# Optimization experiments

Measured on AMD Instinct MI355X. Metric: run time of the kernel, lower is better.

## Reference

```python
import jax, jax.numpy as jnp
import numpy as np

B, N, D, L = 16, 100, 1024, 2000


def setup_inputs() -> dict:
    key = jax.random.key(0)
    ks = jax.random.split(key, 9)
    s = 1.0 / np.sqrt(D)
    return {
        "feature": jax.random.normal(ks[0], (B, N, D), dtype=jnp.float32),
        "graph": jax.random.randint(ks[1], (B, N, N), 0, L),
        "W0": jax.random.normal(ks[2], (D, D), dtype=jnp.float32) * s,
        "W1": jax.random.normal(ks[3], (D, D), dtype=jnp.float32) * s,
        "bias": jax.random.uniform(ks[4], (L, D), dtype=jnp.float32, minval=-s, maxval=s),
        "dp_Wa": jax.random.normal(ks[5], (D, D), dtype=jnp.float32) * s,
        "dp_ba": jax.random.normal(ks[6], (D,), dtype=jnp.float32) * s,
        "dp_Wb": jax.random.normal(ks[7], (D, D), dtype=jnp.float32) * s,
        "dp_bb": jax.random.normal(ks[8], (D,), dtype=jnp.float32) * s,
        "get_alpha": 0,
    }


def reference(feature, graph, W0, W1, bias, dp_Wa, dp_ba, dp_Wb, dp_bb, get_alpha):
    # ---- DirectedGraphConv.conv ----
    adj = (graph != 0).astype(feature.dtype)                     # [B,N,N]
    out = feature + feature @ W0.T + feature @ W1.T              # [B,N,D]
    out = out + jnp.take(bias, graph, axis=0).sum(axis=2)        # label-embedding gather+sum over neighbors
    # ---- relation_alpha: DotProduct(feature, feature) ----
    a = feature @ dp_Wa.T + dp_ba                                # [B,N,D]
    b = feature @ dp_Wb.T + dp_bb                                # [B,N,D]
    alpha = jnp.einsum('bik,bjk->bij', a, b)                     # [B,N,N]
    alpha = jnp.maximum(alpha, 0.0)                              # alpha[alpha<0]=0
    alpha = jnp.einsum('bij,bjk->bik', adj, alpha)               # bmm(adj, alpha)
    alpha = jax.nn.softmax(alpha, axis=1)                        # Softmax(dim=1)
    out = jnp.einsum('bij,bjk->bik', alpha, out)                 # bmm(alpha, output)
    if get_alpha:
        return (out, alpha)
    return out
```

## Files before the change

kernel.cpp:

```cpp
#include <hip/hip_runtime.h>
#include <stdint.h>

#define B_   16
#define N_   100
#define D_   1024
#define L_   2000
#define M_   1600
#define KP   2048
#define AK   3072

#define RCAP 24
#define DCAP 32
#define ZMAX 2400
#define TC   6

typedef __bf16 bf16x8 __attribute__((ext_vector_type(8)));
typedef float  f32x4  __attribute__((ext_vector_type(4)));

__device__ __forceinline__ void gl_lds16(const __bf16* g, __bf16* l) {
    __builtin_amdgcn_global_load_lds(
        (const __attribute__((address_space(1))) void*)g,
        (__attribute__((address_space(3))) void*)l, 16, 0, 0);
}


__global__ void __launch_bounds__(256)
k_prep(const float* __restrict__ f,
       const float* __restrict__ W0, const float* __restrict__ W1,
       const float* __restrict__ Wa, const float* __restrict__ Wb,
       const float* __restrict__ bias, const int* __restrict__ graph,
       __bf16* __restrict__ Acat, __bf16* __restrict__ B0cat,
       __bf16* __restrict__ wcat12, int* __restrict__ colZ) {
    int bid = blockIdx.x, t = threadIdx.x;
    __shared__ float lds[32][33];
    __shared__ unsigned int hist[KP];

    if (bid < 2336) {
        int i = bid * 256 + t;
        union { __bf16 h[8]; uint4 u; } pk;
        if (i < 204800) {
            long base = (long)i * 8;
            const float4* p = (const float4*)(f + base);
            float4 x = p[0], y = p[1];
            pk.h[0]=(__bf16)x.x; pk.h[1]=(__bf16)x.y; pk.h[2]=(__bf16)x.z; pk.h[3]=(__bf16)x.w;
            pk.h[4]=(__bf16)y.x; pk.h[5]=(__bf16)y.y; pk.h[6]=(__bf16)y.z; pk.h[7]=(__bf16)y.w;
            int m = i >> 7, c = i & 127;
            ((uint4*)Acat)[(long)m * 384 + c] = pk.u;
        } else {
            int j = i - 204800;
            long base = (long)j * 8;
            long seg = base >> 20;
            int  js  = j & 131071;
            if (seg == 0) {
                long off = (long)js * 8;
                const float4* p0 = (const float4*)(W0 + off);
                const float4* p1 = (const float4*)(W1 + off);
                float4 a0 = p0[0], a1 = p0[1], b0 = p1[0], b1 = p1[1];
                pk.h[0]=(__bf16)(a0.x+b0.x); pk.h[1]=(__bf16)(a0.y+b0.y);
                pk.h[2]=(__bf16)(a0.z+b0.z); pk.h[3]=(__bf16)(a0.w+b0.w);
                pk.h[4]=(__bf16)(a1.x+b1.x); pk.h[5]=(__bf16)(a1.y+b1.y);
                pk.h[6]=(__bf16)(a1.z+b1.z); pk.h[7]=(__bf16)(a1.w+b1.w);
                int row = js >> 7, c = js & 127;
                ((uint4*)B0cat)[(long)row * 384 + c] = pk.u;
            } else {
                const float* src = (seg == 1) ? Wa : Wb;
                long off = (long)js * 8;
                const float4* p = (const float4*)(src + off);
                float4 x = p[0], y = p[1];
                pk.h[0]=(__bf16)x.x; pk.h[1]=(__bf16)x.y; pk.h[2]=(__bf16)x.z; pk.h[3]=(__bf16)x.w;
                pk.h[4]=(__bf16)y.x; pk.h[5]=(__bf16)y.y; pk.h[6]=(__bf16)y.z; pk.h[7]=(__bf16)y.w;
                ((uint4*)wcat12)[(long)(seg - 1) * 131072 + js] = pk.u;
            }
        }
    } else if (bid < 4384) {
        int tb = bid - 2336;
        int lt = tb >> 5, dt = tb & 31;
        int l0 = lt * 32, d0 = dt * 32;
        int r = t >> 3, cq = (t & 7) * 4;
        float4 v = make_float4(0.f, 0.f, 0.f, 0.f);
        if (l0 + r < L_) v = *(const float4*)(bias + (long)(l0 + r) * D_ + d0 + cq);
        lds[r][cq]=v.x; lds[r][cq+1]=v.y; lds[r][cq+2]=v.z; lds[r][cq+3]=v.w;
        __syncthreads();
        union { __bf16 h[4]; uint2 u; } pk;
        #pragma unroll
        for (int q = 0; q < 4; ++q) pk.h[q] = (__bf16)lds[cq + q][r];
        *(uint2*)(B0cat + (long)(d0 + r) * AK + 1024 + l0 + cq) = pk.u;
    } else if (bid < 5984) {
        int m = bid - 4384;
        for (int k = t; k < KP; k += 256) hist[k] = 0u;
        __syncthreads();
        if (t < N_) atomicAdd(&hist[graph[(long)m * N_ + t]], 1u);
        __syncthreads();
        union { __bf16 h[8]; uint4 u; } pk;
        #pragma unroll
        for (int q = 0; q < 8; ++q) pk.h[q] = (__bf16)(float)hist[t * 8 + q];
        ((uint4*)(Acat + (long)m * AK + 1024))[t] = pk.u;
    } else {
        int b = bid - 5984;
        if (t < N_) {
            const int* g = graph + (long)b * N_ * N_;
            int c = 0;
            for (int i = 0; i < N_; ++i) c += (g[i * N_ + t] == 0);
            colZ[b * N_ + t] = c;
        }
    }
}


#define BM 64
#define BN 128
#define BK 64

__global__ void __launch_bounds__(256)
k_gemmAll(const __bf16* __restrict__ Acat, const __bf16* __restrict__ B0cat,
          const __bf16* __restrict__ wcat12, const int* __restrict__ colZ,
          const float* __restrict__ feat, const float* __restrict__ ba,
          const float* __restrict__ bbias,
          float* __restrict__ out0, float* __restrict__ out0b, float* __restrict__ out0c,
          float* __restrict__ bB, float* __restrict__ aD) {
    __shared__ __align__(16) __bf16 As[BM * BK];
    __shared__ __align__(16) __bf16 Bs[BN * BK];
    __shared__ int czL[2 * N_];
    __shared__ int dcolL[2][DCAP];
    int t = threadIdx.x;
    int pid = blockIdx.x;
    int lane = t & 63, wave = t >> 6;
    int wr = wave & 1, wc = wave >> 1;
    int lrow = lane & 15, quad = lane >> 4;

    int kind, chunk = 0, bm, bn;
    long ldb, koff = 0;
    const __bf16 *Bg;
    if (pid < 600) {
        kind = 0; chunk = pid / 200;
        int p = pid - chunk * 200;
        int v = (p & 7) * 25 + (p >> 3);
        bm = v >> 3; bn = v & 7;
        koff = (long)chunk * 1024;
        Bg = B0cat + (long)(bn * BN) * AK + koff;
        ldb = AK;
    } else if (pid < 800) {
        kind = 1;
        int p = pid - 600;
        int v = (p & 7) * 25 + (p >> 3);
        bm = v >> 3; bn = v & 7;
        Bg = wcat12 + (long)(1024 + bn * BN) * 1024;
        ldb = 1024;
    } else {
        kind = 2;
        int p = pid - 800;
        bn = p & 7; bm = p >> 3;
        Bg = wcat12 + (long)(bn * BN) * 1024;
        ldb = 1024;
        if (t < 2 * N_) czL[t] = colZ[bm * 2 * N_ + t];
        __syncthreads();
        if (t < 2) {
            int rank = 0;
            for (int j = 0; j < N_; ++j)
                if (czL[t * N_ + j] > 0 && rank < DCAP) dcolL[t][rank++] = j;
            for (; rank < DCAP; ++rank) dcolL[t][rank] = 0;
        }
        __syncthreads();
    }

    int r0 = t >> 3, r1 = 32 + (t >> 3);
    int c0 = (t & 7) ^ (r0 & 7), c1 = (t & 7) ^ (r1 & 7);
    const __bf16 *aS0, *aS1;
    if (kind == 2) {
        int b0g = bm * 2 + (r0 >> 5), s0 = r0 & 31;
        int b1g = bm * 2 + (r1 >> 5), s1 = r1 & 31;
        aS0 = Acat + (long)(b0g * N_ + dcolL[r0 >> 5][s0]) * AK + c0 * 8;
        aS1 = Acat + (long)(b1g * N_ + dcolL[r1 >> 5][s1]) * AK + c1 * 8;
    } else {
        aS0 = Acat + (long)(bm * BM + r0) * AK + koff + c0 * 8;
        aS1 = Acat + (long)(bm * BM + r1) * AK + koff + c1 * 8;
    }
    const __bf16 *bS[4];
    #pragma unroll
    for (int pi = 0; pi < 4; ++pi) {
        int rb = pi * 32 + (t >> 3), cb = (t & 7) ^ (rb & 7);
        bS[pi] = Bg + (long)rb * ldb + cb * 8;
    }

    f32x4 acc[2][4] = {};
    for (int k0 = 0; k0 < 1024; k0 += BK) {
        gl_lds16(aS0 + k0, As + t * 8);
        gl_lds16(aS1 + k0, As + (256 + t) * 8);
        #pragma unroll
        for (int pi = 0; pi < 4; ++pi)
            gl_lds16(bS[pi] + k0, Bs + (pi * 256 + t) * 8);
        __syncthreads();
        #pragma unroll
        for (int ks = 0; ks < 2; ++ks) {
            bf16x8 af[2], bf[4];
            #pragma unroll
            for (int i = 0; i < 2; ++i) {
                int r = wr * 32 + i * 16 + lrow;
                int slot = r * 8 + (((ks << 2) | quad) ^ (r & 7));
                af[i] = *(const bf16x8*)(As + slot * 8);
            }
            #pragma unroll
            for (int j = 0; j < 4; ++j) {
                int r = wc * 64 + j * 16 + lrow;
                int slot = r * 8 + (((ks << 2) | quad) ^ (r & 7));
                bf[j] = *(const bf16x8*)(Bs + slot * 8);
            }
            #pragma unroll
            for (int i = 0; i < 2; ++i)
                #pragma unroll
                for (int j = 0; j < 4; ++j)
                    acc[i][j] = __builtin_amdgcn_mfma_f32_16x16x32_bf16(af[i], bf[j], acc[i][j], 0, 0, 0);
        }
        __syncthreads();
    }

    #pragma unroll
    for (int i = 0; i < 2; ++i) {
        int gm0 = bm * BM + wr * 32 + i * 16 + quad * 4;
        #pragma unroll
        for (int j = 0; j < 4; ++j) {
            int col = bn * BN + wc * 64 + j * 16 + lrow;
            #pragma unroll
            for (int r = 0; r < 4; ++r) {
                long m = gm0 + r;
                float v = acc[i][j][r];
                if (kind == 0) {
                    if (chunk == 0)      out0[m * D_ + col]  = v + feat[m * D_ + col];
                    else if (chunk == 1) out0b[m * D_ + col] = v;
                    else                 out0c[m * D_ + col] = v;
                } else if (kind == 1) bB[m * D_ + col] = v + bbias[col];
                else                  aD[m * D_ + col] = v + ba[col];
            }
        }
    }
}


__global__ void __launch_bounds__(256)
k_alpha(const int* __restrict__ graph, const __bf16* __restrict__ Acat,
        const int* __restrict__ colZ, const float* __restrict__ aD,
        const float* __restrict__ bB, float* __restrict__ wl, float* __restrict__ cwG) {
    __shared__ int rowCnt[N_], rowOff[N_], rowRank[N_];
    __shared__ int czA[N_], colSlotL[N_];
    __shared__ int ndvS, totZS;
    __shared__ int zjL[ZMAX];
    __shared__ short prL[ZMAX];
    __shared__ float corrL[RCAP][4];
    __shared__ float wred[4][4];

    int pid = blockIdx.x;
    int b = pid / 25, kc = pid - b * 25;
    int t = threadIdx.x, lane = t & 63, wave = t >> 6;

    const int* g = graph + (long)b * N_ * N_;
    if (t < N_) {
        rowCnt[t] = (int)(float)Acat[(long)(b * N_ + t) * AK + 1024];
        czA[t] = colZ[b * N_ + t];
    }
    if (t < RCAP * 4) corrL[t >> 2][t & 3] = 0.f;
    __syncthreads();
    if (t == 0) {
        int off = 0, rank = 0;
        for (int i = 0; i < N_; ++i) {
            if (rowCnt[i] > 0 && rank < RCAP) {
                rowRank[i] = rank; rowOff[i] = off; off += rowCnt[i]; ++rank;
            } else rowRank[i] = -1;
        }
        ndvS = rank; totZS = off;
    }
    if (t == 64) {
        int ds = 0;
        for (int j = 0; j < N_; ++j) {
            if (czA[j] > 0) { colSlotL[j] = (ds < DCAP) ? ds : 0; ++ds; }
            else colSlotL[j] = -1;
        }
    }
    __syncthreads();
    if (t < N_ && rowRank[t] >= 0) {
        int pos = rowOff[t], r = rowRank[t];
        for (int j = 0; j < N_; ++j)
            if (g[t * N_ + j] == 0) { zjL[pos] = j; prL[pos] = (short)r; ++pos; }
    }
    __syncthreads();
    int Z = totZS, ndv = ndvS;

    int k0 = kc * 4;
    float4 bv[4];
    #pragma unroll
    for (int kk = 0; kk < 4; ++kk)
        bv[kk] = *(const float4*)(bB + ((long)(b * N_ + k0 + kk)) * D_ + t * 4);

    for (int q = 0; q < Z; ++q) {
        int slot = colSlotL[zjL[q]];
        const float* ar = aD + ((long)(b * DCAP + slot)) * D_;
        float4 av = *(const float4*)(ar + t * 4);
        float s[4];
        #pragma unroll
        for (int kk = 0; kk < 4; ++kk)
            s[kk] = av.x * bv[kk].x + av.y * bv[kk].y + av.z * bv[kk].z + av.w * bv[kk].w;
        #pragma unroll
        for (int off = 32; off > 0; off >>= 1)
            #pragma unroll
            for (int kk = 0; kk < 4; ++kk) s[kk] += __shfl_xor(s[kk], off);
        if (lane == 0) { wred[wave][0]=s[0]; wred[wave][1]=s[1]; wred[wave][2]=s[2]; wred[wave][3]=s[3]; }
        __syncthreads();
        if (t < 4) {
            float v = wred[0][t] + wred[1][t] + wred[2][t] + wred[3][t];
            corrL[prL[q]][t] += fmaxf(v, 0.f);
        }
        __syncthreads();
    }

    if (t < 4) {
        int k = k0 + t;
        float denom = (float)(N_ - ndv);
        for (int r = 0; r < ndv; ++r) {
            float e = __expf(-corrL[r][t]);
            corrL[r][t] = e;
            denom += e;
        }
        float w = 1.f / denom;
        wl[b * N_ + k] = w;
        for (int r = 0; r < ndv; ++r)
            cwG[((long)b * RCAP + r) * N_ + k] = corrL[r][t] * w;
    }
}


__global__ void __launch_bounds__(256)
k_mix(const __bf16* __restrict__ Acat, const float* __restrict__ wl,
      const float* __restrict__ cwG, const float* __restrict__ out0,
      const float* __restrict__ out0b, const float* __restrict__ out0c,
      float* __restrict__ out) {
    int b = blockIdx.x, dq = blockIdx.y;
    int t = threadIdx.x, c4 = t & 15, q = t >> 4;
    int d0 = dq * 64;
    __shared__ int hasZ[N_], mapL[N_], ndvS;
    __shared__ float wT[TC][N_];
    __shared__ f32x4 parts[16][TC][16];

    if (t < N_)
        hasZ[t] = ((float)Acat[(long)(b * N_ + t) * AK + 1024] > 0.f) ? 1 : 0;
    __syncthreads();
    if (t < N_) {
        int rank = 0;
        for (int i = 0; i < t; ++i) rank += hasZ[i];
        mapL[t] = (hasZ[t] && rank < RCAP) ? 1 + rank : 0;
    }
    if (t == 0) {
        int n = 0;
        for (int i = 0; i < N_; ++i) n += hasZ[i];
        ndvS = min(n, RCAP);
    }
    __syncthreads();
    int ndv = ndvS, ntask = ndv + 1;

    const float* o0 = out0  + (long)b * N_ * D_ + d0;
    const float* ob = out0b + (long)b * N_ * D_ + d0;
    const float* oc = out0c + (long)b * N_ * D_ + d0;
    for (int cb = 0; cb < ntask; cb += TC) {
        for (int idx = t; idx < TC * N_; idx += 256) {
            int rr = idx / N_, j = idx - rr * N_;
            int task = cb + rr;
            float v = 0.f;
            if (task == 0)         v = wl[b * N_ + j];
            else if (task <= ndv)  v = cwG[((long)b * RCAP + task - 1) * N_ + j];
            wT[rr][j] = v;
        }
        __syncthreads();
        f32x4 acc[TC] = {};
        for (int j = q; j < N_; j += 16) {
            f32x4 v = *(const f32x4*)(o0 + (long)j * D_ + c4 * 4)
                    + *(const f32x4*)(ob + (long)j * D_ + c4 * 4)
                    + *(const f32x4*)(oc + (long)j * D_ + c4 * 4);
            #pragma unroll
            for (int rr = 0; rr < TC; ++rr) acc[rr] += wT[rr][j] * v;
        }
        #pragma unroll
        for (int rr = 0; rr < TC; ++rr) parts[q][rr][c4] = acc[rr];
        __syncthreads();
        for (int i = q; i < N_; i += 16) {
            int task = mapL[i];
            if (task >= cb && task < cb + TC) {
                int rr = task - cb;
                f32x4 s = parts[0][rr][c4];
                #pragma unroll
                for (int p = 1; p < 16; ++p) s += parts[p][rr][c4];
                *(f32x4*)(out + ((long)(b * N_ + i)) * D_ + d0 + c4 * 4) = s;
            }
        }
        __syncthreads();
    }
}


extern "C" void kernel_launch(void* const* d_in, const int* in_sizes, int n_in,
                              void* d_out, int out_size, void* d_ws, size_t ws_size,
                              hipStream_t stream) {
    const float* feature = (const float*)d_in[0];
    const int*   graph   = (const int*)d_in[1];
    const float* W0      = (const float*)d_in[2];
    const float* W1      = (const float*)d_in[3];
    const float* bias    = (const float*)d_in[4];
    const float* dp_Wa   = (const float*)d_in[5];
    const float* dp_ba   = (const float*)d_in[6];
    const float* dp_Wb   = (const float*)d_in[7];
    const float* dp_bb   = (const float*)d_in[8];
    float* out = (float*)d_out;

    char* w = (char*)d_ws;
    __bf16* Acat   = (__bf16*)(w);
    __bf16* B0cat  = (__bf16*)(w + 9830400);
    __bf16* wcat12 = (__bf16*)(w + 16121856);
    float*  out0   = (float*)(w + 20316160);
    float*  out0b  = (float*)(w + 26869760);
    float*  out0c  = (float*)(w + 33423360);
    float*  bB     = (float*)(w + 39976960);
    float*  aD     = (float*)(w + 46530560);
    float*  wl     = (float*)(w + 48627712);
    float*  cwG    = (float*)(w + 48634112);
    int*    colZ   = (int*)  (w + 48787712);

    k_prep<<<6000, 256, 0, stream>>>(feature, W0, W1, dp_Wa, dp_Wb, bias, graph,
                                     Acat, B0cat, wcat12, colZ);
    k_gemmAll<<<864, 256, 0, stream>>>(Acat, B0cat, wcat12, colZ, feature, dp_ba, dp_bb,
                                       out0, out0b, out0c, bB, aD);
    k_alpha<<<400, 256, 0, stream>>>(graph, Acat, colZ, aD, bB, wl, cwG);
    k_mix<<<dim3(B_, 16), 256, 0, stream>>>(Acat, wl, cwG, out0, out0b, out0c, out);
}
```

Measured before the change: 163.8 us.

## Enlarge GEMM M-tile to 128 and fold column zero-count into histogram pass

The GEMM tile grows from 64x128 to 128x128, so each block loads four A row-groups and keeps a 4x4 MFMA accumulator per wave. This roughly halves the grid (448 blocks) and raises reuse of each loaded B tile, with rows padded past M_ and guarded on store. The separate column zero-count blocks are removed; the count is now taken with global atomics inside the histogram blocks after an async memset. The cost is fewer blocks for 256 CUs, higher register pressure, and an extra memset launch.

```diff
diff --git a/kernel.cpp b/kernel.cpp
--- a/kernel.cpp
+++ b/kernel.cpp
@@ -6,6 +6,7 @@
 #define D_   1024
 #define L_   2000
 #define M_   1600
+#define MP   1664
 #define KP   2048
 #define AK   3072
 
@@ -85,29 +86,25 @@
         #pragma unroll
         for (int q = 0; q < 4; ++q) pk.h[q] = (__bf16)lds[cq + q][r];
         *(uint2*)(B0cat + (long)(d0 + r) * AK + 1024 + l0 + cq) = pk.u;
-    } else if (bid < 5984) {
+    } else {
         int m = bid - 4384;
         for (int k = t; k < KP; k += 256) hist[k] = 0u;
         __syncthreads();
-        if (t < N_) atomicAdd(&hist[graph[(long)m * N_ + t]], 1u);
+        if (t < N_) {
+            int gv = graph[(long)m * N_ + t];
+            atomicAdd(&hist[gv], 1u);
+            if (gv == 0) atomicAdd(&colZ[(m / N_) * N_ + t], 1);
+        }
         __syncthreads();
         union { __bf16 h[8]; uint4 u; } pk;
         #pragma unroll
         for (int q = 0; q < 8; ++q) pk.h[q] = (__bf16)(float)hist[t * 8 + q];
         ((uint4*)(Acat + (long)m * AK + 1024))[t] = pk.u;
-    } else {
-        int b = bid - 5984;
-        if (t < N_) {
-            const int* g = graph + (long)b * N_ * N_;
-            int c = 0;
-            for (int i = 0; i < N_; ++i) c += (g[i * N_ + t] == 0);
-            colZ[b * N_ + t] = c;
-        }
-    }
-}
-
-
-#define BM 64
+    }
+}
+
+
+#define BM 128
 #define BN 128
 #define BK 64
 
@@ -120,8 +117,8 @@
           float* __restrict__ bB, float* __restrict__ aD) {
     __shared__ __align__(16) __bf16 As[BM * BK];
     __shared__ __align__(16) __bf16 Bs[BN * BK];
-    __shared__ int czL[2 * N_];
-    __shared__ int dcolL[2][DCAP];
+    __shared__ int czL[4 * N_];
+    __shared__ int dcolL[4][DCAP];
     int t = threadIdx.x;
     int pid = blockIdx.x;
     int lane = t & 63, wave = t >> 6;
@@ -131,30 +128,30 @@
     int kind, chunk = 0, bm, bn;
     long ldb, koff = 0;
     const __bf16 *Bg;
-    if (pid < 600) {
-        kind = 0; chunk = pid / 200;
-        int p = pid - chunk * 200;
-        int v = (p & 7) * 25 + (p >> 3);
+    if (pid < 312) {
+        kind = 0; chunk = pid / 104;
+        int p = pid - chunk * 104;
+        int v = (p & 7) * 13 + (p >> 3);
         bm = v >> 3; bn = v & 7;
         koff = (long)chunk * 1024;
         Bg = B0cat + (long)(bn * BN) * AK + koff;
         ldb = AK;
-    } else if (pid < 800) {
+    } else if (pid < 416) {
         kind = 1;
-        int p = pid - 600;
-        int v = (p & 7) * 25 + (p >> 3);
+        int p = pid - 312;
+        int v = (p & 7) * 13 + (p >> 3);
         bm = v >> 3; bn = v & 7;
         Bg = wcat12 + (long)(1024 + bn * BN) * 1024;
         ldb = 1024;
     } else {
         kind = 2;
-        int p = pid - 800;
+        int p = pid - 416;
         bn = p & 7; bm = p >> 3;
         Bg = wcat12 + (long)(bn * BN) * 1024;
         ldb = 1024;
-        if (t < 2 * N_) czL[t] = colZ[bm * 2 * N_ + t];
-        __syncthreads();
-        if (t < 2) {
+        for (int idx = t; idx < 4 * N_; idx += 256) czL[idx] = colZ[bm * 4 * N_ + idx];
+        __syncthreads();
+        if (t < 4) {
             int rank = 0;
             for (int j = 0; j < N_; ++j)
                 if (czL[t * N_ + j] > 0 && rank < DCAP) dcolL[t][rank++] = j;
@@ -163,39 +160,36 @@
         __syncthreads();
     }
 
-    int r0 = t >> 3, r1 = 32 + (t >> 3);
-    int c0 = (t & 7) ^ (r0 & 7), c1 = (t & 7) ^ (r1 & 7);
-    const __bf16 *aS0, *aS1;
-    if (kind == 2) {
-        int b0g = bm * 2 + (r0 >> 5), s0 = r0 & 31;
-        int b1g = bm * 2 + (r1 >> 5), s1 = r1 & 31;
-        aS0 = Acat + (long)(b0g * N_ + dcolL[r0 >> 5][s0]) * AK + c0 * 8;
-        aS1 = Acat + (long)(b1g * N_ + dcolL[r1 >> 5][s1]) * AK + c1 * 8;
-    } else {
-        aS0 = Acat + (long)(bm * BM + r0) * AK + koff + c0 * 8;
-        aS1 = Acat + (long)(bm * BM + r1) * AK + koff + c1 * 8;
-    }
-    const __bf16 *bS[4];
+    const __bf16 *aS[4], *bS[4];
     #pragma unroll
     for (int pi = 0; pi < 4; ++pi) {
-        int rb = pi * 32 + (t >> 3), cb = (t & 7) ^ (rb & 7);
-        bS[pi] = Bg + (long)rb * ldb + cb * 8;
-    }
-
-    f32x4 acc[2][4] = {};
+        int row = pi * 32 + (t >> 3);
+        int c = (t & 7) ^ (row & 7);
+        if (kind == 2) {
+            int bi = row >> 5, s = row & 31;
+            aS[pi] = Acat + (long)((bm * 4 + bi) * N_ + dcolL[bi][s]) * AK + c * 8;
+        } else {
+            aS[pi] = Acat + (long)(bm * BM + row) * AK + koff + c * 8;
+        }
+        int cb = (t & 7) ^ (row & 7);
+        bS[pi] = Bg + (long)row * ldb + cb * 8;
+    }
+
+    f32x4 acc[4][4] = {};
     for (int k0 = 0; k0 < 1024; k0 += BK) {
-        gl_lds16(aS0 + k0, As + t * 8);
-        gl_lds16(aS1 + k0, As + (256 + t) * 8);
+        #pragma unroll
+        for (int pi = 0; pi < 4; ++pi)
+            gl_lds16(aS[pi] + k0, As + (pi * 256 + t) * 8);
         #pragma unroll
         for (int pi = 0; pi < 4; ++pi)
             gl_lds16(bS[pi] + k0, Bs + (pi * 256 + t) * 8);
         __syncthreads();
         #pragma unroll
         for (int ks = 0; ks < 2; ++ks) {
-            bf16x8 af[2], bf[4];
-            #pragma unroll
-            for (int i = 0; i < 2; ++i) {
-                int r = wr * 32 + i * 16 + lrow;
+            bf16x8 af[4], bf[4];
+            #pragma unroll
+            for (int i = 0; i < 4; ++i) {
+                int r = wr * 64 + i * 16 + lrow;
                 int slot = r * 8 + (((ks << 2) | quad) ^ (r & 7));
                 af[i] = *(const bf16x8*)(As + slot * 8);
             }
@@ -206,7 +200,7 @@
                 bf[j] = *(const bf16x8*)(Bs + slot * 8);
             }
             #pragma unroll
-            for (int i = 0; i < 2; ++i)
+            for (int i = 0; i < 4; ++i)
                 #pragma unroll
                 for (int j = 0; j < 4; ++j)
                     acc[i][j] = __builtin_amdgcn_mfma_f32_16x16x32_bf16(af[i], bf[j], acc[i][j], 0, 0, 0);
@@ -215,8 +209,8 @@
     }
 
     #pragma unroll
-    for (int i = 0; i < 2; ++i) {
-        int gm0 = bm * BM + wr * 32 + i * 16 + quad * 4;
+    for (int i = 0; i < 4; ++i) {
+        int gm0 = bm * BM + wr * 64 + i * 16 + quad * 4;
         #pragma unroll
         for (int j = 0; j < 4; ++j) {
             int col = bn * BN + wc * 64 + j * 16 + lrow;
@@ -225,11 +219,16 @@
                 long m = gm0 + r;
                 float v = acc[i][j][r];
                 if (kind == 0) {
-                    if (chunk == 0)      out0[m * D_ + col]  = v + feat[m * D_ + col];
-                    else if (chunk == 1) out0b[m * D_ + col] = v;
-                    else                 out0c[m * D_ + col] = v;
-                } else if (kind == 1) bB[m * D_ + col] = v + bbias[col];
-                else                  aD[m * D_ + col] = v + ba[col];
+                    if (m < M_) {
+                        if (chunk == 0)      out0[m * D_ + col]  = v + feat[m * D_ + col];
+                        else if (chunk == 1) out0b[m * D_ + col] = v;
+                        else                 out0c[m * D_ + col] = v;
+                    }
+                } else if (kind == 1) {
+                    if (m < M_) bB[m * D_ + col] = v + bbias[col];
+                } else {
+                    aD[m * D_ + col] = v + ba[col];
+                }
             }
         }
     }
@@ -410,20 +409,21 @@
 
     char* w = (char*)d_ws;
     __bf16* Acat   = (__bf16*)(w);
-    __bf16* B0cat  = (__bf16*)(w + 9830400);
-    __bf16* wcat12 = (__bf16*)(w + 16121856);
-    float*  out0   = (float*)(w + 20316160);
-    float*  out0b  = (float*)(w + 26869760);
-    float*  out0c  = (float*)(w + 33423360);
-    float*  bB     = (float*)(w + 39976960);
-    float*  aD     = (float*)(w + 46530560);
-    float*  wl     = (float*)(w + 48627712);
-    float*  cwG    = (float*)(w + 48634112);
-    int*    colZ   = (int*)  (w + 48787712);
-
-    k_prep<<<6000, 256, 0, stream>>>(feature, W0, W1, dp_Wa, dp_Wb, bias, graph,
+    __bf16* B0cat  = (__bf16*)(w + 10223616);
+    __bf16* wcat12 = (__bf16*)(w + 16515072);
+    float*  out0   = (float*)(w + 20709376);
+    float*  out0b  = (float*)(w + 27262976);
+    float*  out0c  = (float*)(w + 33816576);
+    float*  bB     = (float*)(w + 40370176);
+    float*  aD     = (float*)(w + 46923776);
+    float*  wl     = (float*)(w + 49020928);
+    float*  cwG    = (float*)(w + 49027328);
+    int*    colZ   = (int*)  (w + 49180928);
+
+    hipMemsetAsync(colZ, 0, B_ * N_ * sizeof(int), stream);
+    k_prep<<<5984, 256, 0, stream>>>(feature, W0, W1, dp_Wa, dp_Wb, bias, graph,
                                      Acat, B0cat, wcat12, colZ);
-    k_gemmAll<<<864, 256, 0, stream>>>(Acat, B0cat, wcat12, colZ, feature, dp_ba, dp_bb,
+    k_gemmAll<<<448, 256, 0, stream>>>(Acat, B0cat, wcat12, colZ, feature, dp_ba, dp_bb,
                                        out0, out0b, out0c, bB, aD);
     k_alpha<<<400, 256, 0, stream>>>(graph, Acat, colZ, aD, bB, wl, cwG);
     k_mix<<<dim3(B_, 16), 256, 0, stream>>>(Acat, wl, cwG, out0, out0b, out0c, out);
```

New measurement: 172.1 us. 5.0% more time.

## Halve GEMM N-tile to double grid, and coalesce column-zero counting

Applied to the files above, without the earlier changes.

The GEMM tile width drops from 128 to 64 columns, doubling the block count from 864 to 1728 to better fill the GPU's compute units, with block-to-tile mapping and fragment loops updated to match. The column-zero count in the prep kernel now reads graph rows contiguously and accumulates into shared memory with atomics, instead of strided column reads. Smaller tiles lower per-block data reuse and raise total operand traffic. The LDS atomics may contend.

```diff
diff --git a/kernel.cpp b/kernel.cpp
--- a/kernel.cpp
+++ b/kernel.cpp
@@ -97,18 +97,21 @@
         ((uint4*)(Acat + (long)m * AK + 1024))[t] = pk.u;
     } else {
         int b = bid - 5984;
+        const int* g = graph + (long)b * N_ * N_;
+        if (t < N_) hist[t] = 0u;
+        __syncthreads();
         if (t < N_) {
-            const int* g = graph + (long)b * N_ * N_;
-            int c = 0;
-            for (int i = 0; i < N_; ++i) c += (g[i * N_ + t] == 0);
-            colZ[b * N_ + t] = c;
-        }
+            for (int j = 0; j < N_; ++j)
+                if (g[t * N_ + j] == 0) atomicAdd(&hist[j], 1u);
+        }
+        __syncthreads();
+        if (t < N_) colZ[b * N_ + t] = (int)hist[t];
     }
 }
 
 
 #define BM 64
-#define BN 128
+#define BN 64
 #define BK 64
 
 __global__ void __launch_bounds__(256)
@@ -131,25 +134,25 @@
     int kind, chunk = 0, bm, bn;
     long ldb, koff = 0;
     const __bf16 *Bg;
-    if (pid < 600) {
-        kind = 0; chunk = pid / 200;
-        int p = pid - chunk * 200;
-        int v = (p & 7) * 25 + (p >> 3);
-        bm = v >> 3; bn = v & 7;
+    if (pid < 1200) {
+        kind = 0; chunk = pid / 400;
+        int p = pid - chunk * 400;
+        int v = (p & 7) * 50 + (p >> 3);
+        bm = v >> 4; bn = v & 15;
         koff = (long)chunk * 1024;
         Bg = B0cat + (long)(bn * BN) * AK + koff;
         ldb = AK;
-    } else if (pid < 800) {
+    } else if (pid < 1600) {
         kind = 1;
-        int p = pid - 600;
-        int v = (p & 7) * 25 + (p >> 3);
-        bm = v >> 3; bn = v & 7;
+        int p = pid - 1200;
+        int v = (p & 7) * 50 + (p >> 3);
+        bm = v >> 4; bn = v & 15;
         Bg = wcat12 + (long)(1024 + bn * BN) * 1024;
         ldb = 1024;
     } else {
         kind = 2;
-        int p = pid - 800;
-        bn = p & 7; bm = p >> 3;
+        int p = pid - 1600;
+        bm = p >> 4; bn = p & 15;
         Bg = wcat12 + (long)(bn * BN) * 1024;
         ldb = 1024;
         if (t < 2 * N_) czL[t] = colZ[bm * 2 * N_ + t];
@@ -163,36 +166,31 @@
         __syncthreads();
     }
 
-    int r0 = t >> 3, r1 = 32 + (t >> 3);
-    int c0 = (t & 7) ^ (r0 & 7), c1 = (t & 7) ^ (r1 & 7);
-    const __bf16 *aS0, *aS1;
-    if (kind == 2) {
-        int b0g = bm * 2 + (r0 >> 5), s0 = r0 & 31;
-        int b1g = bm * 2 + (r1 >> 5), s1 = r1 & 31;
-        aS0 = Acat + (long)(b0g * N_ + dcolL[r0 >> 5][s0]) * AK + c0 * 8;
-        aS1 = Acat + (long)(b1g * N_ + dcolL[r1 >> 5][s1]) * AK + c1 * 8;
-    } else {
-        aS0 = Acat + (long)(bm * BM + r0) * AK + koff + c0 * 8;
-        aS1 = Acat + (long)(bm * BM + r1) * AK + koff + c1 * 8;
-    }
-    const __bf16 *bS[4];
+    const __bf16 *aS[2], *bS[2];
     #pragma unroll
-    for (int pi = 0; pi < 4; ++pi) {
-        int rb = pi * 32 + (t >> 3), cb = (t & 7) ^ (rb & 7);
-        bS[pi] = Bg + (long)rb * ldb + cb * 8;
-    }
-
-    f32x4 acc[2][4] = {};
+    for (int pi = 0; pi < 2; ++pi) {
+        int row = pi * 32 + (t >> 3);
+        int c = (t & 7) ^ (row & 7);
+        if (kind == 2) {
+            aS[pi] = Acat + (long)((bm * 2 + pi) * N_ + dcolL[pi][t >> 3]) * AK + c * 8;
+        } else {
+            aS[pi] = Acat + (long)(bm * BM + row) * AK + koff + c * 8;
+        }
+        bS[pi] = Bg + (long)row * ldb + c * 8;
+    }
+
+    f32x4 acc[2][2] = {};
     for (int k0 = 0; k0 < 1024; k0 += BK) {
-        gl_lds16(aS0 + k0, As + t * 8);
-        gl_lds16(aS1 + k0, As + (256 + t) * 8);
-        #pragma unroll
-        for (int pi = 0; pi < 4; ++pi)
+        #pragma unroll
+        for (int pi = 0; pi < 2; ++pi)
+            gl_lds16(aS[pi] + k0, As + (pi * 256 + t) * 8);
+        #pragma unroll
+        for (int pi = 0; pi < 2; ++pi)
             gl_lds16(bS[pi] + k0, Bs + (pi * 256 + t) * 8);
         __syncthreads();
         #pragma unroll
         for (int ks = 0; ks < 2; ++ks) {
-            bf16x8 af[2], bf[4];
+            bf16x8 af[2], bf[2];
             #pragma unroll
             for (int i = 0; i < 2; ++i) {
                 int r = wr * 32 + i * 16 + lrow;
@@ -200,15 +198,15 @@
                 af[i] = *(const bf16x8*)(As + slot * 8);
             }
             #pragma unroll
-            for (int j = 0; j < 4; ++j) {
-                int r = wc * 64 + j * 16 + lrow;
+            for (int j = 0; j < 2; ++j) {
+                int r = wc * 32 + j * 16 + lrow;
                 int slot = r * 8 + (((ks << 2) | quad) ^ (r & 7));
                 bf[j] = *(const bf16x8*)(Bs + slot * 8);
             }
             #pragma unroll
             for (int i = 0; i < 2; ++i)
                 #pragma unroll
-                for (int j = 0; j < 4; ++j)
+                for (int j = 0; j < 2; ++j)
                     acc[i][j] = __builtin_amdgcn_mfma_f32_16x16x32_bf16(af[i], bf[j], acc[i][j], 0, 0, 0);
         }
         __syncthreads();
@@ -218,8 +216,8 @@
     for (int i = 0; i < 2; ++i) {
         int gm0 = bm * BM + wr * 32 + i * 16 + quad * 4;
         #pragma unroll
-        for (int j = 0; j < 4; ++j) {
-            int col = bn * BN + wc * 64 + j * 16 + lrow;
+        for (int j = 0; j < 2; ++j) {
+            int col = bn * BN + wc * 32 + j * 16 + lrow;
             #pragma unroll
             for (int r = 0; r < 4; ++r) {
                 long m = gm0 + r;
@@ -423,8 +421,8 @@
 
     k_prep<<<6000, 256, 0, stream>>>(feature, W0, W1, dp_Wa, dp_Wb, bias, graph,
                                      Acat, B0cat, wcat12, colZ);
-    k_gemmAll<<<864, 256, 0, stream>>>(Acat, B0cat, wcat12, colZ, feature, dp_ba, dp_bb,
-                                       out0, out0b, out0c, bB, aD);
+    k_gemmAll<<<1728, 256, 0, stream>>>(Acat, B0cat, wcat12, colZ, feature, dp_ba, dp_bb,
+                                        out0, out0b, out0c, bB, aD);
     k_alpha<<<400, 256, 0, stream>>>(graph, Acat, colZ, aD, bB, wl, cwG);
     k_mix<<<dim3(B_, 16), 256, 0, stream>>>(Acat, wl, cwG, out0, out0b, out0c, out);
 }
```

Measured after the change: 179.1 us. +9.3%, slower.

## Precompute sparse-zero metadata once in prep kernel and share across kernels

Applied to the files above, without the earlier changes.

Moves per-batch metadata building (zero-row ranks, offsets, zero-column slots, packed zero-position lists) into 16 dedicated blocks of the prep kernel. The GEMM, alpha and mix kernels then read these arrays instead of each rebuilding them redundantly; k_alpha previously rebuilt them in all 400 blocks with serial loops. Block order in prep is also rearranged so the slow metadata blocks start first. The risk is that those 16 serial blocks sit on the prep kernel's critical path.

```diff
diff --git a/kernel.cpp b/kernel.cpp
--- a/kernel.cpp
+++ b/kernel.cpp
@@ -30,13 +30,71 @@
        const float* __restrict__ Wa, const float* __restrict__ Wb,
        const float* __restrict__ bias, const int* __restrict__ graph,
        __bf16* __restrict__ Acat, __bf16* __restrict__ B0cat,
-       __bf16* __restrict__ wcat12, int* __restrict__ colZ) {
+       __bf16* __restrict__ wcat12,
+       int* __restrict__ metaNZ, int* __restrict__ metaMap,
+       int* __restrict__ dcolG, int* __restrict__ zprG) {
     int bid = blockIdx.x, t = threadIdx.x;
     __shared__ float lds[32][33];
     __shared__ unsigned int hist[KP];
 
-    if (bid < 2336) {
-        int i = bid * 256 + t;
+    if (bid < 16) {
+        __shared__ int rowCnt_[N_], rowOff_[N_], rowRank_[N_], colSlot_[N_];
+        __shared__ unsigned int colZ_[N_];
+        int b = bid;
+        const int* g = graph + (long)b * N_ * N_;
+        if (t < N_) colZ_[t] = 0u;
+        __syncthreads();
+        if (t < N_) {
+            int rc = 0;
+            for (int j = 0; j < N_; ++j)
+                if (g[t * N_ + j] == 0) { ++rc; atomicAdd(&colZ_[j], 1u); }
+            rowCnt_[t] = rc;
+        }
+        __syncthreads();
+        if (t == 0) {
+            int off = 0, rank = 0;
+            for (int i = 0; i < N_; ++i) {
+                if (rowCnt_[i] > 0 && rank < RCAP) {
+                    rowRank_[i] = rank; rowOff_[i] = off; off += rowCnt_[i]; ++rank;
+                } else rowRank_[i] = -1;
+            }
+            metaNZ[b * 2] = rank; metaNZ[b * 2 + 1] = off;
+        }
+        if (t == 64) {
+            int ds = 0;
+            for (int j = 0; j < N_; ++j) {
+                if (colZ_[j] > 0) {
+                    colSlot_[j] = (ds < DCAP) ? ds : 0;
+                    if (ds < DCAP) dcolG[b * DCAP + ds] = j;
+                    ++ds;
+                } else colSlot_[j] = -1;
+            }
+            for (int s = (ds < DCAP ? ds : DCAP); s < DCAP; ++s) dcolG[b * DCAP + s] = 0;
+        }
+        __syncthreads();
+        if (t < N_) {
+            metaMap[b * N_ + t] = (rowRank_[t] >= 0) ? 1 + rowRank_[t] : 0;
+            if (rowRank_[t] >= 0) {
+                int pos = rowOff_[t], r = rowRank_[t];
+                for (int j = 0; j < N_; ++j)
+                    if (g[t * N_ + j] == 0) {
+                        zprG[b * ZMAX + pos] = r | (colSlot_[j] << 8);
+                        ++pos;
+                    }
+            }
+        }
+    } else if (bid < 1616) {
+        int m = bid - 16;
+        for (int k = t; k < KP; k += 256) hist[k] = 0u;
+        __syncthreads();
+        if (t < N_) atomicAdd(&hist[graph[(long)m * N_ + t]], 1u);
+        __syncthreads();
+        union { __bf16 h[8]; uint4 u; } pk;
+        #pragma unroll
+        for (int q = 0; q < 8; ++q) pk.h[q] = (__bf16)(float)hist[t * 8 + q];
+        ((uint4*)(Acat + (long)m * AK + 1024))[t] = pk.u;
+    } else if (bid < 3952) {
+        int i = (bid - 1616) * 256 + t;
         union { __bf16 h[8]; uint4 u; } pk;
         if (i < 204800) {
             long base = (long)i * 8;
@@ -72,8 +130,8 @@
                 ((uint4*)wcat12)[(long)(seg - 1) * 131072 + js] = pk.u;
             }
         }
-    } else if (bid < 4384) {
-        int tb = bid - 2336;
+    } else {
+        int tb = bid - 3952;
         int lt = tb >> 5, dt = tb & 31;
         int l0 = lt * 32, d0 = dt * 32;
         int r = t >> 3, cq = (t & 7) * 4;
@@ -85,24 +143,6 @@
         #pragma unroll
         for (int q = 0; q < 4; ++q) pk.h[q] = (__bf16)lds[cq + q][r];
         *(uint2*)(B0cat + (long)(d0 + r) * AK + 1024 + l0 + cq) = pk.u;
-    } else if (bid < 5984) {
-        int m = bid - 4384;
-        for (int k = t; k < KP; k += 256) hist[k] = 0u;
-        __syncthreads();
-        if (t < N_) atomicAdd(&hist[graph[(long)m * N_ + t]], 1u);
-        __syncthreads();
-        union { __bf16 h[8]; uint4 u; } pk;
-        #pragma unroll
-        for (int q = 0; q < 8; ++q) pk.h[q] = (__bf16)(float)hist[t * 8 + q];
-        ((uint4*)(Acat + (long)m * AK + 1024))[t] = pk.u;
-    } else {
-        int b = bid - 5984;
-        if (t < N_) {
-            const int* g = graph + (long)b * N_ * N_;
-            int c = 0;
-            for (int i = 0; i < N_; ++i) c += (g[i * N_ + t] == 0);
-            colZ[b * N_ + t] = c;
-        }
     }
 }
 
@@ -113,14 +153,13 @@
 
 __global__ void __launch_bounds__(256)
 k_gemmAll(const __bf16* __restrict__ Acat, const __bf16* __restrict__ B0cat,
-          const __bf16* __restrict__ wcat12, const int* __restrict__ colZ,
+          const __bf16* __restrict__ wcat12, const int* __restrict__ dcolG,
           const float* __restrict__ feat, const float* __restrict__ ba,
           const float* __restrict__ bbias,
           float* __restrict__ out0, float* __restrict__ out0b, float* __restrict__ out0c,
           float* __restrict__ bB, float* __restrict__ aD) {
     __shared__ __align__(16) __bf16 As[BM * BK];
     __shared__ __align__(16) __bf16 Bs[BN * BK];
-    __shared__ int czL[2 * N_];
     __shared__ int dcolL[2][DCAP];
     int t = threadIdx.x;
     int pid = blockIdx.x;
@@ -152,14 +191,7 @@
         bn = p & 7; bm = p >> 3;
         Bg = wcat12 + (long)(bn * BN) * 1024;
         ldb = 1024;
-        if (t < 2 * N_) czL[t] = colZ[bm * 2 * N_ + t];
-        __syncthreads();
-        if (t < 2) {
-            int rank = 0;
-            for (int j = 0; j < N_; ++j)
-                if (czL[t * N_ + j] > 0 && rank < DCAP) dcolL[t][rank++] = j;
-            for (; rank < DCAP; ++rank) dcolL[t][rank] = 0;
-        }
+        if (t < 2 * DCAP) ((int*)dcolL)[t] = dcolG[bm * 2 * DCAP + t];
         __syncthreads();
     }
 
@@ -167,10 +199,8 @@
     int c0 = (t & 7) ^ (r0 & 7), c1 = (t & 7) ^ (r1 & 7);
     const __bf16 *aS0, *aS1;
     if (kind == 2) {
-        int b0g = bm * 2 + (r0 >> 5), s0 = r0 & 31;
-        int b1g = bm * 2 + (r1 >> 5), s1 = r1 & 31;
-        aS0 = Acat + (long)(b0g * N_ + dcolL[r0 >> 5][s0]) * AK + c0 * 8;
-        aS1 = Acat + (long)(b1g * N_ + dcolL[r1 >> 5][s1]) * AK + c1 * 8;
+        aS0 = Acat + (long)((bm * 2 + 0) * N_ + dcolL[0][t >> 3]) * AK + c0 * 8;
+        aS1 = Acat + (long)((bm * 2 + 1) * N_ + dcolL[1][t >> 3]) * AK + c1 * 8;
     } else {
         aS0 = Acat + (long)(bm * BM + r0) * AK + koff + c0 * 8;
         aS1 = Acat + (long)(bm * BM + r1) * AK + koff + c1 * 8;
@@ -237,52 +267,22 @@
 
 
 __global__ void __launch_bounds__(256)
-k_alpha(const int* __restrict__ graph, const __bf16* __restrict__ Acat,
-        const int* __restrict__ colZ, const float* __restrict__ aD,
-        const float* __restrict__ bB, float* __restrict__ wl, float* __restrict__ cwG) {
-    __shared__ int rowCnt[N_], rowOff[N_], rowRank[N_];
-    __shared__ int czA[N_], colSlotL[N_];
-    __shared__ int ndvS, totZS;
-    __shared__ int zjL[ZMAX];
-    __shared__ short prL[ZMAX];
+k_alpha(const int* __restrict__ metaNZ, const int* __restrict__ zprG,
+        const float* __restrict__ aD, const float* __restrict__ bB,
+        float* __restrict__ wl, float* __restrict__ cwG) {
     __shared__ float corrL[RCAP][4];
     __shared__ float wred[4][4];
+    __shared__ int ndvS, ZS;
 
     int pid = blockIdx.x;
     int b = pid / 25, kc = pid - b * 25;
     int t = threadIdx.x, lane = t & 63, wave = t >> 6;
 
-    const int* g = graph + (long)b * N_ * N_;
-    if (t < N_) {
-        rowCnt[t] = (int)(float)Acat[(long)(b * N_ + t) * AK + 1024];
-        czA[t] = colZ[b * N_ + t];
-    }
     if (t < RCAP * 4) corrL[t >> 2][t & 3] = 0.f;
+    if (t == 0) { ndvS = metaNZ[b * 2]; ZS = metaNZ[b * 2 + 1]; }
     __syncthreads();
-    if (t == 0) {
-        int off = 0, rank = 0;
-        for (int i = 0; i < N_; ++i) {
-            if (rowCnt[i] > 0 && rank < RCAP) {
-                rowRank[i] = rank; rowOff[i] = off; off += rowCnt[i]; ++rank;
-            } else rowRank[i] = -1;
-        }
-        ndvS = rank; totZS = off;
-    }
-    if (t == 64) {
-        int ds = 0;
-        for (int j = 0; j < N_; ++j) {
-            if (czA[j] > 0) { colSlotL[j] = (ds < DCAP) ? ds : 0; ++ds; }
-            else colSlotL[j] = -1;
-        }
-    }
-    __syncthreads();
-    if (t < N_ && rowRank[t] >= 0) {
-        int pos = rowOff[t], r = rowRank[t];
-        for (int j = 0; j < N_; ++j)
-            if (g[t * N_ + j] == 0) { zjL[pos] = j; prL[pos] = (short)r; ++pos; }
-    }
-    __syncthreads();
-    int Z = totZS, ndv = ndvS;
+    int Z = ZS, ndv = ndvS;
+    const int* zp = zprG + b * ZMAX;
 
     int k0 = kc * 4;
     float4 bv[4];
@@ -291,7 +291,8 @@
         bv[kk] = *(const float4*)(bB + ((long)(b * N_ + k0 + kk)) * D_ + t * 4);
 
     for (int q = 0; q < Z; ++q) {
-        int slot = colSlotL[zjL[q]];
+        int e = zp[q];
+        int r = e & 255, slot = e >> 8;
         const float* ar = aD + ((long)(b * DCAP + slot)) * D_;
         float4 av = *(const float4*)(ar + t * 4);
         float s[4];
@@ -306,7 +307,7 @@
         __syncthreads();
         if (t < 4) {
             float v = wred[0][t] + wred[1][t] + wred[2][t] + wred[3][t];
-            corrL[prL[q]][t] += fmaxf(v, 0.f);
+            corrL[r][t] += fmaxf(v, 0.f);
         }
         __syncthreads();
     }
@@ -328,30 +329,19 @@
 
 
 __global__ void __launch_bounds__(256)
-k_mix(const __bf16* __restrict__ Acat, const float* __restrict__ wl,
-      const float* __restrict__ cwG, const float* __restrict__ out0,
-      const float* __restrict__ out0b, const float* __restrict__ out0c,
-      float* __restrict__ out) {
+k_mix(const int* __restrict__ metaNZ, const int* __restrict__ metaMap,
+      const float* __restrict__ wl, const float* __restrict__ cwG,
+      const float* __restrict__ out0, const float* __restrict__ out0b,
+      const float* __restrict__ out0c, float* __restrict__ out) {
     int b = blockIdx.x, dq = blockIdx.y;
     int t = threadIdx.x, c4 = t & 15, q = t >> 4;
     int d0 = dq * 64;
-    __shared__ int hasZ[N_], mapL[N_], ndvS;
+    __shared__ int mapL[N_], ndvS;
     __shared__ float wT[TC][N_];
     __shared__ f32x4 parts[16][TC][16];
 
-    if (t < N_)
-        hasZ[t] = ((float)Acat[(long)(b * N_ + t) * AK + 1024] > 0.f) ? 1 : 0;
-    __syncthreads();
-    if (t < N_) {
-        int rank = 0;
-        for (int i = 0; i < t; ++i) rank += hasZ[i];
-        mapL[t] = (hasZ[t] && rank < RCAP) ? 1 + rank : 0;
-    }
-    if (t == 0) {
-        int n = 0;
-        for (int i = 0; i < N_; ++i) n += hasZ[i];
-        ndvS = min(n, RCAP);
-    }
+    if (t < N_) mapL[t] = metaMap[b * N_ + t];
+    if (t == 0) ndvS = metaNZ[b * 2];
     __syncthreads();
     int ndv = ndvS, ntask = ndv + 1;
 
@@ -409,22 +399,25 @@
     float* out = (float*)d_out;
 
     char* w = (char*)d_ws;
-    __bf16* Acat   = (__bf16*)(w);
-    __bf16* B0cat  = (__bf16*)(w + 9830400);
-    __bf16* wcat12 = (__bf16*)(w + 16121856);
-    float*  out0   = (float*)(w + 20316160);
-    float*  out0b  = (float*)(w + 26869760);
-    float*  out0c  = (float*)(w + 33423360);
-    float*  bB     = (float*)(w + 39976960);
-    float*  aD     = (float*)(w + 46530560);
-    float*  wl     = (float*)(w + 48627712);
-    float*  cwG    = (float*)(w + 48634112);
-    int*    colZ   = (int*)  (w + 48787712);
+    __bf16* Acat    = (__bf16*)(w);
+    __bf16* B0cat   = (__bf16*)(w + 9830400);
+    __bf16* wcat12  = (__bf16*)(w + 16121856);
+    float*  out0    = (float*)(w + 20316160);
+    float*  out0b   = (float*)(w + 26869760);
+    float*  out0c   = (float*)(w + 33423360);
+    float*  bB      = (float*)(w + 39976960);
+    float*  aD      = (float*)(w + 46530560);
+    float*  wl      = (float*)(w + 48627712);
+    float*  cwG     = (float*)(w + 48634112);
+    int*    metaNZ  = (int*)  (w + 48787712);
+    int*    metaMap = (int*)  (w + 48787840);
+    int*    dcolG   = (int*)  (w + 48794240);
+    int*    zprG    = (int*)  (w + 48796288);
 
     k_prep<<<6000, 256, 0, stream>>>(feature, W0, W1, dp_Wa, dp_Wb, bias, graph,
-                                     Acat, B0cat, wcat12, colZ);
-    k_gemmAll<<<864, 256, 0, stream>>>(Acat, B0cat, wcat12, colZ, feature, dp_ba, dp_bb,
+                                     Acat, B0cat, wcat12, metaNZ, metaMap, dcolG, zprG);
+    k_gemmAll<<<864, 256, 0, stream>>>(Acat, B0cat, wcat12, dcolG, feature, dp_ba, dp_bb,
                                        out0, out0b, out0c, bB, aD);
-    k_alpha<<<400, 256, 0, stream>>>(graph, Acat, colZ, aD, bB, wl, cwG);
-    k_mix<<<dim3(B_, 16), 256, 0, stream>>>(Acat, wl, cwG, out0, out0b, out0c, out);
-}
+    k_alpha<<<400, 256, 0, stream>>>(metaNZ, zprG, aD, bB, wl, cwG);
+    k_mix<<<dim3(B_, 16), 256, 0, stream>>>(metaNZ, metaMap, wl, cwG, out0, out0b, out0c, out);
+}
```

Result: slower. 168.6 us (+2.9%).
